# Kernel tuning notes

Hardware: AMD Instinct MI355X
Metric: run time of the kernel (lower is better)

## Reference

```python
import jax, jax.numpy as jnp
import numpy as np

D_MODEL = 2048
NUM_Q_HEADS = 32
NUM_KV_HEADS = 8
HEAD_DIM = D_MODEL // NUM_Q_HEADS  # 64
NUM_GROUPS = NUM_Q_HEADS // NUM_KV_HEADS  # 4


def setup_inputs() -> dict:
    key = jax.random.key(0)
    ks = jax.random.split(key, 9)
    s = 1.0 / np.sqrt(D_MODEL)
    x = jax.random.normal(ks[0], (2, 2048, D_MODEL), dtype=jnp.float32)
    Wq = jax.random.uniform(ks[1], (D_MODEL, NUM_Q_HEADS * HEAD_DIM), jnp.float32, -s, s)
    bq = jax.random.uniform(ks[2], (NUM_Q_HEADS * HEAD_DIM,), jnp.float32, -s, s)
    Wk = jax.random.uniform(ks[3], (D_MODEL, NUM_KV_HEADS * HEAD_DIM), jnp.float32, -s, s)
    bk = jax.random.uniform(ks[4], (NUM_KV_HEADS * HEAD_DIM,), jnp.float32, -s, s)
    Wv = jax.random.uniform(ks[5], (D_MODEL, NUM_KV_HEADS * HEAD_DIM), jnp.float32, -s, s)
    bv = jax.random.uniform(ks[6], (NUM_KV_HEADS * HEAD_DIM,), jnp.float32, -s, s)
    Wo = jax.random.uniform(ks[7], (D_MODEL, D_MODEL), jnp.float32, -s, s)
    bo = jax.random.uniform(ks[8], (D_MODEL,), jnp.float32, -s, s)
    return {"x": x, "Wq": Wq, "bq": bq, "Wk": Wk, "bk": bk,
            "Wv": Wv, "bv": bv, "Wo": Wo, "bo": bo}


def reference(x, Wq, bq, Wk, bk, Wv, bv, Wo, bo):
    B, T, C = x.shape
    Hkv, G, Dh = NUM_KV_HEADS, NUM_GROUPS, HEAD_DIM
    # projections
    q = (x @ Wq + bq).reshape(B, T, Hkv, G, Dh)   # group G query heads per kv head
    k = (x @ Wk + bk).reshape(B, T, Hkv, Dh)
    v = (x @ Wv + bv).reshape(B, T, Hkv, Dh)
    scale = 1.0 / np.sqrt(Dh).astype(np.float32)
    # scores: [B, Hkv, G, T, T] (kv head broadcast over its G query heads)
    scores = jnp.einsum('btkgd,bskd->bkgts', q, k) * scale
    attn = jax.nn.softmax(scores, axis=-1)
    out = jnp.einsum('bkgts,bskd->btkgd', attn, v).reshape(B, T, C)
    return out @ Wo + bo
```

## Files before the change

kernel.cpp:

```cpp
#include <hip/hip_runtime.h>
#include <cstdint>
#include <cstddef>
#include <math.h>

typedef uint16_t bf16;
typedef __attribute__((ext_vector_type(8))) __bf16 bf16x8;
typedef __attribute__((ext_vector_type(2))) float f32x2;
typedef __attribute__((ext_vector_type(4))) float f32x4;
typedef __attribute__((ext_vector_type(16))) float f32x16;

#define MFMA16(a,b,c) __builtin_amdgcn_mfma_f32_16x16x32_bf16((a),(b),(c),0,0,0)
#define MFMA32(a,b,c) __builtin_amdgcn_mfma_f32_32x32x16_bf16((a),(b),(c),0,0,0)

__device__ __forceinline__ uint16_t f2bf(float f){
  uint32_t u = __float_as_uint(f);
  return (uint16_t)((u + 0x7fffu + ((u >> 16) & 1u)) >> 16);
}
__device__ __forceinline__ uint32_t pk2(float lo, float hi){
  return (uint32_t)f2bf(lo) | ((uint32_t)f2bf(hi) << 16);
}

__device__ __forceinline__ void gload_lds16(const void* g, void* l){
  __builtin_amdgcn_global_load_lds((const __attribute__((address_space(1))) void*)g,
                                   (__attribute__((address_space(3))) void*)l, 16, 0, 0);
}

__global__ void k_convert(const float* __restrict__ in, bf16* __restrict__ out, int n){
  int i = (blockIdx.x * 256 + threadIdx.x) * 4;
  if (i >= n) return;
  float4 v = *reinterpret_cast<const float4*>(in + i);
  uint32_t lo = pk2(v.x, v.y);
  uint32_t hi = pk2(v.z, v.w);
  uint2 pkv = make_uint2(lo, hi);
  *reinterpret_cast<uint2*>(out + i) = pkv;
}

__global__ void k_transposeW(const float* __restrict__ in, bf16* __restrict__ out, int R, int C){
  __shared__ float tile[64][65];
  int c0 = blockIdx.x * 64, r0 = blockIdx.y * 64;
  int t = threadIdx.x;
  int fx = t & 15, fy = t >> 4;
  #pragma unroll
  for (int i = 0; i < 4; i++){
    int r = fy + i*16;
    float4 v = *reinterpret_cast<const float4*>(in + (size_t)(r0 + r)*C + c0 + fx*4);
    tile[r][fx*4+0] = v.x; tile[r][fx*4+1] = v.y;
    tile[r][fx*4+2] = v.z; tile[r][fx*4+3] = v.w;
  }
  __syncthreads();
  int gx = t & 7, gy = t >> 3;
  #pragma unroll
  for (int i = 0; i < 2; i++){
    int c = gy + i*32;
    int rr = gx*8;
    union { bf16 h[8]; uint4 u; } pk_;
    #pragma unroll
    for (int j = 0; j < 8; j++) pk_.h[j] = f2bf(tile[rr+j][c]);
    *reinterpret_cast<uint4*>(out + (size_t)(c0 + c)*R + r0 + rr) = pk_.u;
  }
}

__device__ __forceinline__ void gemm128_core(
    const bf16* __restrict__ Abase, const bf16* __restrict__ Btbase,
    int lda, int ldb, int K, bf16* As, bf16* Bs, f32x4 acc[4][4])
{
  const int tid = threadIdx.x;
  const int wid = tid >> 6, lane = tid & 63;
  const int wr = wid >> 1, wc = wid & 1;
  const int lr = lane & 15, lg = lane >> 4;
  const f32x4 vzero = {0.f, 0.f, 0.f, 0.f};

  #pragma unroll
  for (int m = 0; m < 4; m++)
    #pragma unroll
    for (int n = 0; n < 4; n++)
      acc[m][n] = vzero;

  int srcA[4], srcB[4], dOff[4];
  #pragma unroll
  for (int i = 0; i < 4; i++){
    int d = i*4096 + wid*1024 + lane*16;
    int row = d >> 7, sp = (d >> 4) & 7;
    int sl = sp ^ (row & 7);
    srcA[i] = row * lda + sl * 8;
    srcB[i] = row * ldb + sl * 8;
    dOff[i] = i*4096 + wid*1024;
  }

  for (int k0 = 0; k0 < K; k0 += 64){
    #pragma unroll
    for (int i = 0; i < 4; i++)
      gload_lds16(Abase + k0 + srcA[i], (char*)As + dOff[i]);
    #pragma unroll
    for (int i = 0; i < 4; i++)
      gload_lds16(Btbase + k0 + srcB[i], (char*)Bs + dOff[i]);
    __syncthreads();
    #pragma unroll
    for (int ks = 0; ks < 2; ks++){
      bf16x8 af[4], bfr[4];
      #pragma unroll
      for (int m = 0; m < 4; m++){
        int row = wr*64 + m*16 + lr;
        int sp = (ks*4 + lg) ^ (row & 7);
        af[m] = *reinterpret_cast<const bf16x8*>(As + row*64 + sp*8);
      }
      #pragma unroll
      for (int n = 0; n < 4; n++){
        int row = wc*64 + n*16 + lr;
        int sp = (ks*4 + lg) ^ (row & 7);
        bfr[n] = *reinterpret_cast<const bf16x8*>(Bs + row*64 + sp*8);
      }
      #pragma unroll
      for (int m = 0; m < 4; m++)
        #pragma unroll
        for (int n = 0; n < 4; n++)
          acc[m][n] = MFMA16(af[m], bfr[n], acc[m][n]);
    }
    __syncthreads();
  }
}

__global__ __launch_bounds__(256, 2) void k_qkv(
    const bf16* __restrict__ xb,
    const bf16* __restrict__ WqT, const bf16* __restrict__ WkT, const bf16* __restrict__ WvT,
    const float* __restrict__ bq, const float* __restrict__ bk, const float* __restrict__ bv,
    bf16* __restrict__ qo, bf16* __restrict__ ko, bf16* __restrict__ vtp)
{
  __shared__ __align__(16) bf16 As[128*64];
  __shared__ __align__(16) bf16 Bs[128*64];
  int by = blockIdx.y;
  const bf16* Bt; const float* bias; int mode; int y = 0; float scale = 1.f;
  if (by < 16){      Bt = WqT + (size_t)by*128*2048;      bias = bq + by*128; mode = 0; y = by;   scale = 0.18033688011112042f; }
  else if (by < 20){ y = by-16; Bt = WkT + (size_t)y*128*2048; bias = bk + y*128; mode = 1; }
  else {             y = by-20; Bt = WvT + (size_t)y*128*2048; bias = bv + y*128; mode = 2; }
  int m0 = blockIdx.x * 128;
  f32x4 acc[4][4];
  gemm128_core(xb + (size_t)m0*2048, Bt, 2048, 2048, 2048, As, Bs, acc);
  const int tid = threadIdx.x, wid = tid >> 6, lane = tid & 63;
  const int wr = wid >> 1, wc = wid & 1, lr = lane & 15, lg = lane >> 4;
  if (mode == 2){
    #pragma unroll
    for (int n = 0; n < 4; n++){
      int cl = wc*64 + n*16 + lr;
      float bb = bias[cl];
      #pragma unroll
      for (int m = 0; m < 4; m++){
        int row0 = m0 + wr*64 + m*16 + lg*4;
        int bi = row0 >> 11, tl = row0 & 2047;
        union { bf16 h[4]; uint2 u; } pk_;
        #pragma unroll
        for (int r = 0; r < 4; r++) pk_.h[r] = f2bf(acc[m][n][r] + bb);
        *reinterpret_cast<uint2*>(vtp + ((size_t)bi*512 + y*128 + cl)*2048 + tl) = pk_.u;
      }
    }
  } else {
    bf16* outp = (mode == 0) ? (qo + y*128) : (ko + y*128);
    int ldc = (mode == 0) ? 2048 : 512;
    #pragma unroll
    for (int n = 0; n < 4; n++){
      int col = wc*64 + n*16 + lr;
      float bb = bias[col];
      #pragma unroll
      for (int m = 0; m < 4; m++)
        #pragma unroll
        for (int r = 0; r < 4; r++){
          int row = m0 + wr*64 + m*16 + lg*4 + r;
          outp[(size_t)row*ldc + col] = f2bf((acc[m][n][r] + bb) * scale);
        }
    }
  }
}

__global__ __launch_bounds__(256, 2) void k_oproj(
    const bf16* __restrict__ ab, const bf16* __restrict__ WoT,
    const float* __restrict__ bo, float* __restrict__ outp)
{
  __shared__ __align__(16) bf16 As[128*64];
  __shared__ __align__(16) bf16 Bs[128*64];
  int m0 = blockIdx.x * 128, n0 = blockIdx.y * 128;
  f32x4 acc[4][4];
  gemm128_core(ab + (size_t)m0*2048, WoT + (size_t)n0*2048, 2048, 2048, 2048, As, Bs, acc);
  const int tid = threadIdx.x, wid = tid >> 6, lane = tid & 63;
  const int wr = wid >> 1, wc = wid & 1, lr = lane & 15, lg = lane >> 4;
  #pragma unroll
  for (int n = 0; n < 4; n++){
    int col = n0 + wc*64 + n*16 + lr;
    float bb = bo[col];
    #pragma unroll
    for (int m = 0; m < 4; m++)
      #pragma unroll
      for (int r = 0; r < 4; r++){
        int row = m0 + wr*64 + m*16 + lg*4 + r;
        outp[(size_t)row*2048 + col] = acc[m][n][r] + bb;
      }
  }
}

__global__ __launch_bounds__(512, 2) void k_flash(
    const bf16* __restrict__ q, const bf16* __restrict__ kmat,
    const bf16* __restrict__ vt, bf16* __restrict__ ao)
{
  __shared__ __align__(16) char lds[65536];
  const int tid = threadIdx.x;
  const int wid = tid >> 6, lane = tid & 63;
  const int l31 = lane & 31, hi = lane >> 5;
  const int bh = blockIdx.y;
  const int b = bh >> 5, hq = bh & 31, kvh = hq >> 2;
  const int qt = blockIdx.x;
  const int qrow0 = b*2048 + qt*512 + wid*64;

  bf16x8 qf[2][4];
  #pragma unroll
  for (int g = 0; g < 2; g++){
    const bf16* qrow = q + (size_t)(qrow0 + g*32 + l31)*2048 + hq*64 + hi*8;
    #pragma unroll
    for (int t = 0; t < 4; t++)
      qf[g][t] = *reinterpret_cast<const bf16x8*>(qrow + t*16);
  }

  f32x16 oacc[2][2];
  #pragma unroll
  for (int g = 0; g < 2; g++)
    #pragma unroll
    for (int n = 0; n < 2; n++)
      #pragma unroll
      for (int r = 0; r < 16; r++) oacc[g][n][r] = 0.f;
  float rsg[2][2];
  rsg[0][0]=0.f; rsg[0][1]=0.f; rsg[1][0]=0.f; rsg[1][1]=0.f;
  const f32x16 zv = {0.f,0.f,0.f,0.f,0.f,0.f,0.f,0.f,0.f,0.f,0.f,0.f,0.f,0.f,0.f,0.f};

  const int r7 = l31 & 7;
  int A[8];
  #pragma unroll
  for (int j = 0; j < 8; j++)
    A[j] = l31*128 + (((2*j + hi) ^ r7) << 4);

  const bf16* kbase = kmat + (size_t)b*2048*512 + kvh*64;
  const bf16* vbase = vt + ((size_t)b*512 + kvh*64)*2048;

  int kSrc[2], vSrc[2];
  const int dOf = wid*1024;
  #pragma unroll
  for (int i = 0; i < 2; i++){
    int kdb = i*8192 + tid*16;
    int krow = kdb >> 7, ksp = (kdb >> 4) & 7, ksl = ksp ^ (krow & 7);
    kSrc[i] = krow*512 + ksl*8;
    int o = tid*16;
    int vrow = o >> 7, vsp = (o >> 4) & 7, vsl = vsp ^ (vrow & 7);
    vSrc[i] = vrow*2048 + i*64 + vsl*8;
  }

  #define STAGE(buf, st_) do { \
    const bf16* kb_ = kbase + (size_t)(st_)*128*512; \
    const bf16* vb_ = vbase + (st_)*128; \
    gload_lds16(kb_ + kSrc[0], lds + (buf)*16384 + dOf); \
    gload_lds16(kb_ + kSrc[1], lds + (buf)*16384 + 8192 + dOf); \
    gload_lds16(vb_ + vSrc[0], lds + 32768 + (buf)*16384 + dOf); \
    gload_lds16(vb_ + vSrc[1], lds + 32768 + (buf)*16384 + 8192 + dOf); \
  } while(0)

  #define LDK(j, imm) (*reinterpret_cast<const bf16x8*>(lds + A[j] + (imm)))
  #define LDV(j, imm) (*reinterpret_cast<const bf16x8*>(lds + A[j] + 32768 + (imm)))

  STAGE(0, 0);
  __syncthreads();

  for (int st = 0; st < 16; st++){
    if (st < 15) STAGE((st & 1)^1, st+1);

    #pragma unroll
    for (int c = 0; c < 2; c++){
      f32x16 sc[2][2];
      __builtin_amdgcn_s_setprio(1);
      #pragma unroll
      for (int t = 0; t < 4; t++){
        bf16x8 af0 = LDK(t, c*8192);
        bf16x8 af1 = LDK(t, c*8192 + 4096);
        if (t == 0){
          sc[0][0] = MFMA32(af0, qf[0][0], zv);
          sc[1][0] = MFMA32(af0, qf[1][0], zv);
          sc[0][1] = MFMA32(af1, qf[0][0], zv);
          sc[1][1] = MFMA32(af1, qf[1][0], zv);
        } else {
          sc[0][0] = MFMA32(af0, qf[0][t], sc[0][0]);
          sc[1][0] = MFMA32(af0, qf[1][t], sc[1][0]);
          sc[0][1] = MFMA32(af1, qf[0][t], sc[0][1]);
          sc[1][1] = MFMA32(af1, qf[1][t], sc[1][1]);
        }
      }
      __builtin_amdgcn_s_setprio(0);

      uint32_t pw[2][2][8];
      #pragma unroll
      for (int g = 0; g < 2; g++){
        #pragma unroll
        for (int n = 0; n < 2; n++)
          #pragma unroll
          for (int j = 0; j < 8; j++){
            float plo = __builtin_amdgcn_exp2f(sc[g][n][2*j]);
            float phi = __builtin_amdgcn_exp2f(sc[g][n][2*j+1]);
            rsg[g][j & 1] += plo + phi;
            asm("v_cvt_pk_bf16_f32 %0, %1, %2" : "=v"(pw[g][n][j]) : "v"(plo), "v"(phi));
          }
        #pragma unroll
        for (int n = 0; n < 2; n++)
          #pragma unroll
          for (int h = 0; h < 2; h++){
            asm volatile("v_permlane32_swap_b32 %0, %1" : "+v"(pw[g][n][h*4+0]), "+v"(pw[g][n][h*4+2]));
            asm volatile("v_permlane32_swap_b32 %0, %1" : "+v"(pw[g][n][h*4+1]), "+v"(pw[g][n][h*4+3]));
          }
      }

      __builtin_amdgcn_s_setprio(1);
      #pragma unroll
      for (int kk = 0; kk < 4; kk++){
        int n = kk >> 1, h = kk & 1;
        union { uint32_t w[4]; bf16x8 v; } pa0, pa1;
        #pragma unroll
        for (int w_ = 0; w_ < 4; w_++){ pa0.w[w_] = pw[0][n][h*4+w_]; pa1.w[w_] = pw[1][n][h*4+w_]; }
        #pragma unroll
        for (int nd = 0; nd < 2; nd++){
          bf16x8 vf = LDV(kk, c*8192 + nd*4096);
          oacc[0][nd] = MFMA32(pa0.v, vf, oacc[0][nd]);
          oacc[1][nd] = MFMA32(pa1.v, vf, oacc[1][nd]);
        }
      }
      __builtin_amdgcn_s_setprio(0);
    }
    __syncthreads();
    #pragma unroll
    for (int j = 0; j < 8; j++) A[j] ^= 16384;
  }
  #undef STAGE
  #undef LDK
  #undef LDV

  #pragma unroll
  for (int g = 0; g < 2; g++){
    float rs = rsg[g][0] + rsg[g][1];
    float l = rs + __shfl_xor(rs, 32);
    float linv = 1.f / l;
    float lv[16];
    #pragma unroll
    for (int r = 0; r < 16; r++){
      int qi = (r & 3) + 8*(r >> 2) + 4*hi;
      lv[r] = __shfl(linv, qi);
    }
    #pragma unroll
    for (int nd = 0; nd < 2; nd++)
      #pragma unroll
      for (int r = 0; r < 16; r++){
        int qi = (r & 3) + 8*(r >> 2) + 4*hi;
        int row = qrow0 + g*32 + qi;
        ao[(size_t)row*2048 + hq*64 + nd*32 + l31] = f2bf(oacc[g][nd][r] * lv[r]);
      }
  }
}

extern "C" void kernel_launch(void* const* d_in, const int* in_sizes, int n_in,
                              void* d_out, int out_size, void* d_ws, size_t ws_size,
                              hipStream_t stream)
{
  const float* x  = (const float*)d_in[0];
  const float* Wq = (const float*)d_in[1];
  const float* bq = (const float*)d_in[2];
  const float* Wk = (const float*)d_in[3];
  const float* bk = (const float*)d_in[4];
  const float* Wv = (const float*)d_in[5];
  const float* bv = (const float*)d_in[6];
  const float* Wo = (const float*)d_in[7];
  const float* bo = (const float*)d_in[8];
  float* out = (float*)d_out;

  char* ws = (char*)d_ws;
  size_t off = 0;
  auto alloc = [&](size_t bytes){ char* p = ws + off; off += (bytes + 255) & ~(size_t)255; return p; };
  bf16* xb  = (bf16*)alloc(2*2048*2048*2);
  bf16* WqT = (bf16*)alloc(2048*2048*2);
  bf16* WkT = (bf16*)alloc(512*2048*2);
  bf16* WvT = (bf16*)alloc(512*2048*2);
  bf16* WoT = (bf16*)alloc(2048*2048*2);
  bf16* qb  = (bf16*)alloc(4096*2048*2);
  bf16* kb  = (bf16*)alloc((size_t)4096*512*2);
  bf16* vtb = (bf16*)alloc((size_t)4096*512*2);
  bf16* aob = xb;

  k_convert<<<8192, 256, 0, stream>>>(x, xb, 2*2048*2048);
  k_transposeW<<<dim3(32,32), 256, 0, stream>>>(Wq, WqT, 2048, 2048);
  k_transposeW<<<dim3(8,32),  256, 0, stream>>>(Wk, WkT, 2048, 512);
  k_transposeW<<<dim3(8,32),  256, 0, stream>>>(Wv, WvT, 2048, 512);
  k_transposeW<<<dim3(32,32), 256, 0, stream>>>(Wo, WoT, 2048, 2048);
  k_qkv<<<dim3(32,24), 256, 0, stream>>>(xb, WqT, WkT, WvT, bq, bk, bv, qb, kb, vtb);
  k_flash<<<dim3(4,64), 512, 0, stream>>>(qb, kb, vtb, aob);
  k_oproj<<<dim3(32,16), 256, 0, stream>>>(aob, WoT, bo, out);
}
```

Before: 193.0 us.

## Triple-buffer K/V tiles in flash attention with explicit vmcnt waits

```diff
diff --git a/kernel.cpp b/kernel.cpp
--- a/kernel.cpp
+++ b/kernel.cpp
@@ -200,7 +200,7 @@
     const bf16* __restrict__ q, const bf16* __restrict__ kmat,
     const bf16* __restrict__ vt, bf16* __restrict__ ao)
 {
-  __shared__ __align__(16) char lds[65536];
+  __shared__ __align__(16) char lds[98304];
   const int tid = threadIdx.x;
   const int wid = tid >> 6, lane = tid & 63;
   const int l31 = lane & 31, hi = lane >> 5;
@@ -230,9 +230,9 @@
   const f32x16 zv = {0.f,0.f,0.f,0.f,0.f,0.f,0.f,0.f,0.f,0.f,0.f,0.f,0.f,0.f,0.f,0.f};
 
   const int r7 = l31 & 7;
-  int A[8];
-  #pragma unroll
-  for (int j = 0; j < 8; j++)
+  int A[4];
+  #pragma unroll
+  for (int j = 0; j < 4; j++)
     A[j] = l31*128 + (((2*j + hi) ^ r7) << 4);
 
   const bf16* kbase = kmat + (size_t)b*2048*512 + kvh*64;
@@ -250,23 +250,33 @@
     vSrc[i] = vrow*2048 + i*64 + vsl*8;
   }
 
-  #define STAGE(buf, st_) do { \
+  #define STAGE(bo, st_) do { \
     const bf16* kb_ = kbase + (size_t)(st_)*128*512; \
     const bf16* vb_ = vbase + (st_)*128; \
-    gload_lds16(kb_ + kSrc[0], lds + (buf)*16384 + dOf); \
-    gload_lds16(kb_ + kSrc[1], lds + (buf)*16384 + 8192 + dOf); \
-    gload_lds16(vb_ + vSrc[0], lds + 32768 + (buf)*16384 + dOf); \
-    gload_lds16(vb_ + vSrc[1], lds + 32768 + (buf)*16384 + 8192 + dOf); \
+    gload_lds16(kb_ + kSrc[0], lds + (bo) + dOf); \
+    gload_lds16(kb_ + kSrc[1], lds + (bo) + 8192 + dOf); \
+    gload_lds16(vb_ + vSrc[0], lds + 49152 + (bo) + dOf); \
+    gload_lds16(vb_ + vSrc[1], lds + 49152 + (bo) + 8192 + dOf); \
   } while(0)
 
-  #define LDK(j, imm) (*reinterpret_cast<const bf16x8*>(lds + A[j] + (imm)))
-  #define LDV(j, imm) (*reinterpret_cast<const bf16x8*>(lds + A[j] + 32768 + (imm)))
+  #define LDK(j, imm) (*reinterpret_cast<const bf16x8*>(lds + kOff + A[j] + (imm)))
+  #define LDV(j, imm) (*reinterpret_cast<const bf16x8*>(lds + 49152 + kOff + A[j] + (imm)))
 
   STAGE(0, 0);
-  __syncthreads();
-
+  STAGE(16384, 1);
+
+  int kOff = 0;
+  int sOff = 32768;
   for (int st = 0; st < 16; st++){
-    if (st < 15) STAGE((st & 1)^1, st+1);
+    if (st == 15) asm volatile("s_waitcnt vmcnt(0)" ::: "memory");
+    else          asm volatile("s_waitcnt vmcnt(4)" ::: "memory");
+    __builtin_amdgcn_sched_barrier(0);
+    __builtin_amdgcn_s_barrier();
+    __builtin_amdgcn_sched_barrier(0);
+    if (st < 14){
+      STAGE(sOff, st+2);
+      sOff = (sOff == 32768) ? 0 : sOff + 16384;
+    }
 
     #pragma unroll
     for (int c = 0; c < 2; c++){
@@ -327,9 +337,7 @@
       }
       __builtin_amdgcn_s_setprio(0);
     }
-    __syncthreads();
-    #pragma unroll
-    for (int j = 0; j < 8; j++) A[j] ^= 16384;
+    kOff = (kOff == 32768) ? 0 : kOff + 16384;
   }
   #undef STAGE
   #undef LDK
```

New measurement: 193.8 us. Within noise of the previous version (+0.4%).
